# Kernel tuning notes

Hardware: AMD Instinct MI355X
Metric: run time of the kernel (lower is better)

The kernel has to match this reference:

```python
import jax, jax.numpy as jnp
import numpy as np

KS, STRIDE, PAD, GROUPS = 7, 1, 3, 8


def setup_inputs() -> dict:
    key = jax.random.key(0)
    ks = jax.random.split(key, 6)
    B, C, H, W = 4, 128, 64, 64
    O = 128
    rel_size = O // GROUPS // 2  # 8
    return {
        "x": jax.random.normal(ks[0], (B, C, H, W), jnp.float32),
        "wq": jax.random.normal(ks[1], (O, C), jnp.float32) * 0.05,
        "wk": jax.random.normal(ks[2], (O, C), jnp.float32) * 0.05,
        "wv": jax.random.normal(ks[3], (O, C), jnp.float32) * 0.05,
        "rel_x": jax.random.normal(ks[4], (rel_size, KS), jnp.float32),
        "rel_y": jax.random.normal(ks[5], (O // GROUPS - rel_size, KS), jnp.float32),
    }


def _patches(a, fH, fW):
    # a: [B, C, pH, pW] -> [B, C, fH, fW, KS, KS] (overlapping windows, like torch unfold)
    cols = []
    for ki in range(KS):
        rows = []
        for kj in range(KS):
            rows.append(a[:, :, ki:ki + (fH - 1) * STRIDE + 1:STRIDE,
                             kj:kj + (fW - 1) * STRIDE + 1:STRIDE])
        cols.append(jnp.stack(rows, axis=-1))  # last axis = l (W-kernel)
    return jnp.stack(cols, axis=-2)            # second-to-last = k (H-kernel)


def reference(x, wq, wk, wv, rel_x, rel_y):
    B, C, H, W = x.shape
    O = wq.shape[0]
    rel_size = rel_x.shape[0]
    xp = jnp.pad(x, ((0, 0), (0, 0), (PAD, PAD), (PAD, PAD)))
    pH, pW = H + 2 * PAD, W + 2 * PAD
    fH, fW = (pH - KS) // STRIDE + 1, (pW - KS) // STRIDE + 1
    # 1x1 convs
    q = jnp.einsum('oc,bchw->bohw', wq, xp)
    k = jnp.einsum('oc,bchw->bohw', wk, xp)
    v = jnp.einsum('oc,bchw->bohw', wv, xp)
    h0 = (KS - 1) // 2
    win_q = q[:, :, h0:pH - KS // 2:STRIDE, h0:pW - KS // 2:STRIDE]  # [B,O,fH,fW]
    win_q_b = win_q.reshape(B, GROUPS, O // GROUPS, fH, fW)
    qx = win_q_b[:, :, :rel_size]
    qy = win_q_b[:, :, rel_size:]
    bias_x = jnp.einsum('bgxhw,xk->bhwk', qx, rel_x)  # varies along l (W-kernel)
    bias_y = jnp.einsum('bgyhw,yk->bhwk', qy, rel_y)  # varies along k (H-kernel)
    win_k = _patches(k, fH, fW)  # [B,O,fH,fW,KS,KS]
    win_v = _patches(v, fH, fW)
    logits = jnp.einsum('bchw,bchwkl->bhwkl', win_q, win_k)
    logits = logits + bias_x[:, :, :, None, :] + bias_y[:, :, :, :, None]
    attn = jax.nn.softmax(logits.reshape(B, fH, fW, KS * KS), axis=-1)
    attn = attn.reshape(B, fH, fW, KS, KS)
    out = jnp.einsum('bhwkl,bchwkl->bchw', attn, win_v)  # [B,O,fH,fW]
    return out
```

## Files before the change

### kernel.cpp

```cpp
#include <hip/hip_runtime.h>

typedef __fp16 half8_t __attribute__((ext_vector_type(8)));
typedef __fp16 h2_t    __attribute__((ext_vector_type(2)));
typedef float  f4_t    __attribute__((ext_vector_type(4)));

constexpr int CI = 128, HW = 4096;

__device__ __forceinline__ h2_t u2h(unsigned u) { return __builtin_bit_cast(h2_t, u); }
__device__ __forceinline__ float dot2(unsigned k, unsigned q, float c) {
#if __has_builtin(__builtin_amdgcn_fdot2)
    return __builtin_amdgcn_fdot2(u2h(k), u2h(q), c, false);
#else
    h2_t kh = u2h(k), qh = u2h(q);
    return c + (float)kh[0] * (float)qh[0] + (float)kh[1] * (float)qh[1];
#endif
}

__global__ __launch_bounds__(256) void prepass(
    const float* __restrict__ x, const float* __restrict__ wq,
    const float* __restrict__ wk, const float* __restrict__ wv,
    __fp16* __restrict__ xh, __fp16* __restrict__ wh)
{
    const int tid = threadIdx.x, bx = blockIdx.x;
    const int wvn = tid >> 6, lane = tid & 63;
    const int quad = lane >> 4, n = lane & 15;
    if (bx < 1024) {
        const int t = bx, ck = wvn;
        const int p = t * 16 + n, b = p >> 12, hw = p & 4095;
        const float* src = x + (size_t)b * (CI * HW) + (size_t)(ck * 32 + quad * 8) * HW + hw;
        half8_t hv;
#pragma unroll
        for (int j = 0; j < 8; ++j) hv[j] = (__fp16)src[(size_t)j * HW];
        *(half8_t*)(xh + ((size_t)((t * 4 + ck) * 64 + lane)) * 8) = hv;
    } else {
        const int item = (bx - 1024) * 4 + wvn;
        const int g = item >> 3, ot = (item >> 2) & 1, ck = item & 3;
        const int mtx = g >> 2, olb = (g & 3) * 32;
        const float* wsrc = (mtx == 0) ? wq : (mtx == 1 ? wk : wv);
        const float* row = wsrc + (size_t)(olb + ot * 16 + n) * CI + ck * 32 + quad * 8;
        half8_t hv;
#pragma unroll
        for (int j = 0; j < 8; ++j) hv[j] = (__fp16)row[j];
        *(half8_t*)(wh + ((size_t)(item * 64 + lane)) * 8) = hv;
    }
}

__global__ __launch_bounds__(256) void qkv_mfma(
    const __fp16* __restrict__ xh, const __fp16* __restrict__ wh,
    unsigned* __restrict__ qf, unsigned* __restrict__ kf, unsigned* __restrict__ vf)
{
    __shared__ float tlds[4][16 * 17];
    const int tid = threadIdx.x, wvn = tid >> 6, lane = tid & 63;
    const int g = blockIdx.x;
    const int m = lane & 15, quad = lane >> 4;
    unsigned* dst = (g < 4) ? qf : (g < 8 ? kf : vf);
    const int c2base = (g & 3) * 16;

    half8_t A[2][4];
#pragma unroll
    for (int ot = 0; ot < 2; ++ot)
#pragma unroll
        for (int ck = 0; ck < 4; ++ck)
            A[ot][ck] = *(const half8_t*)(wh + ((size_t)((((g * 2 + ot) * 4 + ck) * 64 + lane)) * 8));

    float* tl = tlds[wvn];
    const int t0 = blockIdx.y * 16 + wvn * 4;
    for (int ti = 0; ti < 4; ++ti) {
        const int t = t0 + ti;
        half8_t B[4];
#pragma unroll
        for (int ck = 0; ck < 4; ++ck)
            B[ck] = *(const half8_t*)(xh + ((size_t)((t * 4 + ck) * 64 + lane)) * 8);
        const int p0 = t * 16;
#pragma unroll
        for (int ot = 0; ot < 2; ++ot) {
            f4_t acc = {0.f, 0.f, 0.f, 0.f};
#pragma unroll
            for (int ck = 0; ck < 4; ++ck)
                acc = __builtin_amdgcn_mfma_f32_16x16x32_f16(A[ot][ck], B[ck], acc, 0, 0, 0);
            const int c2l = ot * 8 + quad * 2;
            tl[m * 17 + c2l]     = __builtin_bit_cast(float, __builtin_amdgcn_cvt_pkrtz(acc[0], acc[1]));
            tl[m * 17 + c2l + 1] = __builtin_bit_cast(float, __builtin_amdgcn_cvt_pkrtz(acc[2], acc[3]));
        }
        __asm__ volatile("s_waitcnt lgkmcnt(0)" ::: "memory");
        __builtin_amdgcn_wave_barrier();
#pragma unroll
        for (int s = 0; s < 4; ++s) {
            const int px = s * 4 + quad, c2l = m;
            dst[(size_t)(p0 + px) * 64 + c2base + c2l] =
                __builtin_bit_cast(unsigned, tl[px * 17 + c2l]);
        }
        __builtin_amdgcn_wave_barrier();
    }
}

__global__ __launch_bounds__(512) void attn_kernel(
    const unsigned* __restrict__ qf, const unsigned* __restrict__ kf,
    const unsigned* __restrict__ vf, const float* __restrict__ relx,
    const float* __restrict__ rely, float* __restrict__ out)
{
    __shared__ unsigned smem[15232];
    unsigned* kS   = smem;
    unsigned* vS   = smem + 7296;
    float*    rels = (float*)(smem + 14592);
    float*    sxyL = (float*)(smem + 14704);
    float*    biasL= (float*)(smem + 14976);
    float*    otile= (float*)smem;

    const int tid = threadIdx.x, bx = blockIdx.x;
    const int wv = tid >> 6, lane = tid & 63;
    const int w0 = (bx & 7) * 8;
    const int h0 = ((bx >> 3) & 31) * 2;
    const int b  = bx >> 8;
    const int dr = wv >> 2, dw0 = (wv & 3) * 2;
    const int pixbase = b * 4096 + (h0 + dr) * 64 + (w0 + dw0);

    if (tid < 112) rels[tid] = (tid < 56) ? relx[tid] : rely[tid - 56];

#pragma unroll
    for (int it = 0; it < 14; ++it) {
        int idx = it * 512 + tid;
        const int isv = idx >= 3584;
        idx -= isv * 3584;
        const int pos = idx >> 5, c2 = (idx & 31) * 2;
        const int ri = pos / 14, ci = pos - ri * 14;
        const int r = h0 - 3 + ri, cw = w0 - 3 + ci;
        uint2 d = make_uint2(0u, 0u);
        if ((unsigned)r < 64u && (unsigned)cw < 64u) {
            const unsigned* src = isv ? vf : kf;
            d = *(const uint2*)(src + (size_t)((b * 4096 + r * 64 + cw) * 64 + c2));
        }
        unsigned* dstS = isv ? vS : kS;
        dstS[c2 * 114 + pos]       = d.x;
        dstS[(c2 + 1) * 114 + pos] = d.y;
    }

    if (lane < 32) {
        const int px01 = lane >> 4, t = lane & 15;
        const int pix = pixbase + px01;
        float s = 0.f;
#pragma unroll
        for (int gg = 0; gg < 8; ++gg) {
            const h2_t hh = u2h(qf[(size_t)pix * 64 + gg * 8 + (t >> 1)]);
            s += (float)hh[t & 1];
        }
        sxyL[(wv * 2 + px01) * 17 + t] = s;
    }
    __syncthreads();

    if (lane < 28) {
        const int px01 = lane >= 14;
        const int j = lane - px01 * 14;
        const int isy = j >= 7;
        const int jj = j - isy * 7;
        const float* sx = &sxyL[(wv * 2 + px01) * 17 + isy * 8];
        const float* rl = &rels[isy * 56 + jj];
        float s = 0.f;
#pragma unroll
        for (int i = 0; i < 8; ++i) s += sx[i] * rl[i * 7];
        biasL[(wv * 2 + px01) * 16 + j] = s;
    }
    __syncthreads();

    const int nn = (lane < 49) ? lane : 48;
    const int ki = (nn * 37) >> 8, kj = nn - ki * 7;
    int apk[2];
#pragma unroll
    for (int px01 = 0; px01 < 2; ++px01) {
        const int pixu = __builtin_amdgcn_readfirstlane(pixbase + px01);
        const uint4* qp = (const uint4*)(qf + (size_t)pixu * 64);
        const int pos = (dr + ki) * 14 + (dw0 + px01 + kj);
        float acc = 0.f;
#pragma unroll
        for (int c4 = 0; c4 < 16; ++c4) {
            const uint4 qw = qp[c4];
            acc = dot2(kS[(c4 * 4 + 0) * 114 + pos], qw.x, acc);
            acc = dot2(kS[(c4 * 4 + 1) * 114 + pos], qw.y, acc);
            acc = dot2(kS[(c4 * 4 + 2) * 114 + pos], qw.z, acc);
            acc = dot2(kS[(c4 * 4 + 3) * 114 + pos], qw.w, acc);
        }
        const float* bb = &biasL[(wv * 2 + px01) * 16];
        float logit = (lane < 49) ? acc + bb[kj] + bb[7 + ki] : -1e30f;
        float mx = logit;
#pragma unroll
        for (int off = 32; off; off >>= 1) mx = fmaxf(mx, __shfl_xor(mx, off));
        const float e = __expf(logit - mx);
        float ss = e;
#pragma unroll
        for (int off = 32; off; off >>= 1) ss += __shfl_xor(ss, off);
        const float a = e / ss;
        apk[px01] = __builtin_bit_cast(int, __builtin_amdgcn_cvt_pkrtz(a, a));
    }
    __syncthreads();

    const int posb = dr * 14 + dw0;
    h2_t o0 = {(__fp16)0.f, (__fp16)0.f}, o1 = o0;
#pragma unroll
    for (int n = 0; n < 49; ++n) {
        const int nki = (n * 37) >> 8, nkj = n - nki * 7;
        const int p = posb + nki * 14 + nkj;
        const unsigned va = vS[lane * 114 + p];
        const unsigned vb = vS[lane * 114 + p + 1];
        const h2_t a0 = u2h((unsigned)__builtin_amdgcn_readlane(apk[0], n));
        const h2_t a1 = u2h((unsigned)__builtin_amdgcn_readlane(apk[1], n));
        o0 += a0 * u2h(va);
        o1 += a1 * u2h(vb);
    }
    const int pxl0 = dr * 8 + dw0;
    {
        float2 f0 = make_float2((float)o0[0], (float)o0[1]);
        float2 f1 = make_float2((float)o1[0], (float)o1[1]);
        *(float2*)&otile[(size_t)pxl0 * 130 + lane * 2]       = f0;
        *(float2*)&otile[(size_t)(pxl0 + 1) * 130 + lane * 2] = f1;
    }
    __syncthreads();

#pragma unroll
    for (int s = 0; s < 4; ++s) {
        const int i = s * 512 + tid;
        const int c = i >> 4, pxl = i & 15;
        const int drr = pxl >> 3, dww = pxl & 7;
        out[(size_t)(b * 128 + c) * 4096 + (h0 + drr) * 64 + (w0 + dww)] =
            otile[pxl * 130 + c];
    }
}

extern "C" void kernel_launch(void* const* d_in, const int* in_sizes, int n_in,
                              void* d_out, int out_size, void* d_ws, size_t ws_size,
                              hipStream_t stream) {
    const float* x    = (const float*)d_in[0];
    const float* wq   = (const float*)d_in[1];
    const float* wk   = (const float*)d_in[2];
    const float* wv   = (const float*)d_in[3];
    const float* relx = (const float*)d_in[4];
    const float* rely = (const float*)d_in[5];
    float* out = (float*)d_out;

    char* ws = (char*)d_ws;
    __fp16*   xh = (__fp16*)(ws);
    __fp16*   wh = (__fp16*)(ws + 0x400000);
    unsigned* qf = (unsigned*)(ws + 0x420000);
    unsigned* kf = (unsigned*)(ws + 0x820000);
    unsigned* vf = (unsigned*)(ws + 0xC20000);

    prepass<<<dim3(1048), 256, 0, stream>>>(x, wq, wk, wv, xh, wh);
    qkv_mfma<<<dim3(12, 64), 256, 0, stream>>>(xh, wh, qf, kf, vf);
    attn_kernel<<<dim3(1024), 512, 0, stream>>>(qf, kf, vf, relx, rely, out);
}
```

Measured before the change: 106.1 us.

## Fuse fp16 conversion into QKV MFMA kernel and enlarge attention tiles

Removes the separate prepass that converted x and weights to fp16. The QKV projection kernel now converts weights into LDS and x into registers itself, and each block computes one full matrix for 64 pixels. The attention kernel moves to 1024-thread blocks covering 4x8 pixels, which shrinks the halo overhead of the K/V staging. It also interleaves the two pixels' dot products per wave. In exchange, each QKV block re-reads and re-converts the whole weight matrix, x is read three times (once per Q/K/V), and the larger LDS footprint may lower occupancy.

New measurement: 103.3 us. 2.6% less time.

```diff
diff --git a/kernel.cpp b/kernel.cpp
--- a/kernel.cpp
+++ b/kernel.cpp
@@ -3,8 +3,6 @@
 typedef __fp16 half8_t __attribute__((ext_vector_type(8)));
 typedef __fp16 h2_t    __attribute__((ext_vector_type(2)));
 typedef float  f4_t    __attribute__((ext_vector_type(4)));
-
-constexpr int CI = 128, HW = 4096;
 
 __device__ __forceinline__ h2_t u2h(unsigned u) { return __builtin_bit_cast(h2_t, u); }
 __device__ __forceinline__ float dot2(unsigned k, unsigned q, float c) {
@@ -15,114 +13,107 @@
     return c + (float)kh[0] * (float)qh[0] + (float)kh[1] * (float)qh[1];
 #endif
 }
-
-__global__ __launch_bounds__(256) void prepass(
+__device__ __forceinline__ unsigned pk(float a, float b) {
+    return __builtin_bit_cast(unsigned, __builtin_amdgcn_cvt_pkrtz(a, b));
+}
+
+__global__ __launch_bounds__(256) void qkv_fused(
     const float* __restrict__ x, const float* __restrict__ wq,
     const float* __restrict__ wk, const float* __restrict__ wv,
-    __fp16* __restrict__ xh, __fp16* __restrict__ wh)
+    unsigned* __restrict__ qf, unsigned* __restrict__ kf,
+    unsigned* __restrict__ vf)
 {
-    const int tid = threadIdx.x, bx = blockIdx.x;
-    const int wvn = tid >> 6, lane = tid & 63;
-    const int quad = lane >> 4, n = lane & 15;
-    if (bx < 1024) {
-        const int t = bx, ck = wvn;
-        const int p = t * 16 + n, b = p >> 12, hw = p & 4095;
-        const float* src = x + (size_t)b * (CI * HW) + (size_t)(ck * 32 + quad * 8) * HW + hw;
-        half8_t hv;
-#pragma unroll
-        for (int j = 0; j < 8; ++j) hv[j] = (__fp16)src[(size_t)j * HW];
-        *(half8_t*)(xh + ((size_t)((t * 4 + ck) * 64 + lane)) * 8) = hv;
-    } else {
-        const int item = (bx - 1024) * 4 + wvn;
-        const int g = item >> 3, ot = (item >> 2) & 1, ck = item & 3;
-        const int mtx = g >> 2, olb = (g & 3) * 32;
-        const float* wsrc = (mtx == 0) ? wq : (mtx == 1 ? wk : wv);
-        const float* row = wsrc + (size_t)(olb + ot * 16 + n) * CI + ck * 32 + quad * 8;
-        half8_t hv;
-#pragma unroll
-        for (int j = 0; j < 8; ++j) hv[j] = (__fp16)row[j];
-        *(half8_t*)(wh + ((size_t)(item * 64 + lane)) * 8) = hv;
-    }
-}
-
-__global__ __launch_bounds__(256) void qkv_mfma(
-    const __fp16* __restrict__ xh, const __fp16* __restrict__ wh,
-    unsigned* __restrict__ qf, unsigned* __restrict__ kf, unsigned* __restrict__ vf)
-{
-    __shared__ float tlds[4][16 * 17];
+    __shared__ __fp16 Af[2048 * 8];
+    __shared__ float  tl4[4][16 * 17];
+
     const int tid = threadIdx.x, wvn = tid >> 6, lane = tid & 63;
-    const int g = blockIdx.x;
+    const int mtx = blockIdx.x >> 8;
+    const int tg  = blockIdx.x & 255;
+    const float* wsrc = (mtx == 0) ? wq : (mtx == 1 ? wk : wv);
+    unsigned*    dst  = (mtx == 0) ? qf : (mtx == 1 ? kf : vf);
+
+#pragma unroll
+    for (int s = 0; s < 8; ++s) {
+        const int it = s * 256 + tid;
+        const int l = it & 63, ck = (it >> 6) & 3, ot = it >> 8;
+        const float* wr = wsrc + (size_t)(ot * 16 + (l & 15)) * 128 + ck * 32 + (l >> 4) * 8;
+        const float4 w0 = *(const float4*)wr;
+        const float4 w1 = *(const float4*)(wr + 4);
+        half8_t h;
+        h[0] = (__fp16)w0.x; h[1] = (__fp16)w0.y; h[2] = (__fp16)w0.z; h[3] = (__fp16)w0.w;
+        h[4] = (__fp16)w1.x; h[5] = (__fp16)w1.y; h[6] = (__fp16)w1.z; h[7] = (__fp16)w1.w;
+        *(half8_t*)&Af[it * 8] = h;
+    }
+
+    const int t = tg * 4 + wvn;
     const int m = lane & 15, quad = lane >> 4;
-    unsigned* dst = (g < 4) ? qf : (g < 8 ? kf : vf);
-    const int c2base = (g & 3) * 16;
-
-    half8_t A[2][4];
-#pragma unroll
-    for (int ot = 0; ot < 2; ++ot)
-#pragma unroll
-        for (int ck = 0; ck < 4; ++ck)
-            A[ot][ck] = *(const half8_t*)(wh + ((size_t)((((g * 2 + ot) * 4 + ck) * 64 + lane)) * 8));
-
-    float* tl = tlds[wvn];
-    const int t0 = blockIdx.y * 16 + wvn * 4;
-    for (int ti = 0; ti < 4; ++ti) {
-        const int t = t0 + ti;
-        half8_t B[4];
-#pragma unroll
-        for (int ck = 0; ck < 4; ++ck)
-            B[ck] = *(const half8_t*)(xh + ((size_t)((t * 4 + ck) * 64 + lane)) * 8);
-        const int p0 = t * 16;
+    const int p0 = t * 16, b = p0 >> 12, hw = p0 & 4095;
+    const float* xb = x + (size_t)b * (128 * 4096) + hw + m;
+    half8_t B[4];
+#pragma unroll
+    for (int ck = 0; ck < 4; ++ck) {
+        half8_t h;
+#pragma unroll
+        for (int j = 0; j < 8; ++j)
+            h[j] = (__fp16)xb[(size_t)(ck * 32 + quad * 8 + j) * 4096];
+        B[ck] = h;
+    }
+    __syncthreads();
+
+    float* tl = tl4[wvn];
+#pragma unroll
+    for (int og = 0; og < 4; ++og) {
 #pragma unroll
         for (int ot = 0; ot < 2; ++ot) {
+            const int otile = og * 2 + ot;
             f4_t acc = {0.f, 0.f, 0.f, 0.f};
 #pragma unroll
-            for (int ck = 0; ck < 4; ++ck)
-                acc = __builtin_amdgcn_mfma_f32_16x16x32_f16(A[ot][ck], B[ck], acc, 0, 0, 0);
+            for (int ck = 0; ck < 4; ++ck) {
+                const half8_t A = *(const half8_t*)&Af[((otile * 4 + ck) * 64 + lane) * 8];
+                acc = __builtin_amdgcn_mfma_f32_16x16x32_f16(A, B[ck], acc, 0, 0, 0);
+            }
             const int c2l = ot * 8 + quad * 2;
-            tl[m * 17 + c2l]     = __builtin_bit_cast(float, __builtin_amdgcn_cvt_pkrtz(acc[0], acc[1]));
-            tl[m * 17 + c2l + 1] = __builtin_bit_cast(float, __builtin_amdgcn_cvt_pkrtz(acc[2], acc[3]));
+            tl[m * 17 + c2l]     = __builtin_bit_cast(float, pk(acc[0], acc[1]));
+            tl[m * 17 + c2l + 1] = __builtin_bit_cast(float, pk(acc[2], acc[3]));
         }
         __asm__ volatile("s_waitcnt lgkmcnt(0)" ::: "memory");
         __builtin_amdgcn_wave_barrier();
 #pragma unroll
         for (int s = 0; s < 4; ++s) {
-            const int px = s * 4 + quad, c2l = m;
-            dst[(size_t)(p0 + px) * 64 + c2base + c2l] =
-                __builtin_bit_cast(unsigned, tl[px * 17 + c2l]);
+            const int px = s * 4 + quad;
+            dst[(size_t)(p0 + px) * 64 + og * 16 + m] =
+                __builtin_bit_cast(unsigned, tl[px * 17 + m]);
         }
         __builtin_amdgcn_wave_barrier();
     }
 }
 
-__global__ __launch_bounds__(512) void attn_kernel(
+__global__ __launch_bounds__(1024) void attn_kernel(
     const unsigned* __restrict__ qf, const unsigned* __restrict__ kf,
     const unsigned* __restrict__ vf, const float* __restrict__ relx,
     const float* __restrict__ rely, float* __restrict__ out)
 {
-    __shared__ unsigned smem[15232];
-    unsigned* kS   = smem;
-    unsigned* vS   = smem + 7296;
-    float*    rels = (float*)(smem + 14592);
-    float*    sxyL = (float*)(smem + 14704);
-    float*    biasL= (float*)(smem + 14976);
-    float*    otile= (float*)smem;
+    __shared__ unsigned smem[19472];
+    unsigned* kS    = smem;
+    unsigned* vS    = smem + 9152;
+    float*    rels  = (float*)(smem + 18304);
+    float*    sxyL  = (float*)(smem + 18416);
+    float*    biasL = (float*)(smem + 18960);
+    float*    otile = (float*)smem;
 
     const int tid = threadIdx.x, bx = blockIdx.x;
     const int wv = tid >> 6, lane = tid & 63;
     const int w0 = (bx & 7) * 8;
-    const int h0 = ((bx >> 3) & 31) * 2;
-    const int b  = bx >> 8;
+    const int h0 = ((bx >> 3) & 15) * 4;
+    const int b  = bx >> 7;
     const int dr = wv >> 2, dw0 = (wv & 3) * 2;
-    const int pixbase = b * 4096 + (h0 + dr) * 64 + (w0 + dw0);
 
     if (tid < 112) rels[tid] = (tid < 56) ? relx[tid] : rely[tid - 56];
 
-#pragma unroll
-    for (int it = 0; it < 14; ++it) {
-        int idx = it * 512 + tid;
-        const int isv = idx >= 3584;
-        idx -= isv * 3584;
-        const int pos = idx >> 5, c2 = (idx & 31) * 2;
+    for (int i = tid; i < 8960; i += 1024) {
+        const int isv = i >= 4480;
+        const int ii  = i - isv * 4480;
+        const int pos = ii >> 5, c2 = (ii & 31) * 2;
         const int ri = pos / 14, ci = pos - ri * 14;
         const int r = h0 - 3 + ri, cw = w0 - 3 + ci;
         uint2 d = make_uint2(0u, 0u);
@@ -131,56 +122,62 @@
             d = *(const uint2*)(src + (size_t)((b * 4096 + r * 64 + cw) * 64 + c2));
         }
         unsigned* dstS = isv ? vS : kS;
-        dstS[c2 * 114 + pos]       = d.x;
-        dstS[(c2 + 1) * 114 + pos] = d.y;
-    }
-
-    if (lane < 32) {
-        const int px01 = lane >> 4, t = lane & 15;
-        const int pix = pixbase + px01;
+        dstS[c2 * 143 + pos]       = d.x;
+        dstS[(c2 + 1) * 143 + pos] = d.y;
+    }
+
+    if (tid < 512) {
+        const int px = tid >> 4, tt = tid & 15;
+        const int pix = b * 4096 + (h0 + (px >> 3)) * 64 + w0 + (px & 7);
         float s = 0.f;
 #pragma unroll
-        for (int gg = 0; gg < 8; ++gg) {
-            const h2_t hh = u2h(qf[(size_t)pix * 64 + gg * 8 + (t >> 1)]);
-            s += (float)hh[t & 1];
-        }
-        sxyL[(wv * 2 + px01) * 17 + t] = s;
-    }
-    __syncthreads();
-
-    if (lane < 28) {
-        const int px01 = lane >= 14;
-        const int j = lane - px01 * 14;
-        const int isy = j >= 7;
-        const int jj = j - isy * 7;
-        const float* sx = &sxyL[(wv * 2 + px01) * 17 + isy * 8];
+        for (int g = 0; g < 8; ++g) {
+            const h2_t hh = u2h(qf[(size_t)pix * 64 + g * 8 + (tt >> 1)]);
+            s += (float)hh[tt & 1];
+        }
+        sxyL[px * 17 + tt] = s;
+    }
+    __syncthreads();
+
+    if (tid < 448) {
+        const int px = tid / 14, j = tid - px * 14;
+        const int isy = j >= 7, jj = j - isy * 7;
+        const float* sx = &sxyL[px * 17 + isy * 8];
         const float* rl = &rels[isy * 56 + jj];
         float s = 0.f;
 #pragma unroll
-        for (int i = 0; i < 8; ++i) s += sx[i] * rl[i * 7];
-        biasL[(wv * 2 + px01) * 16 + j] = s;
+        for (int i = 0; i < 8; ++i) s = fmaf(sx[i], rl[i * 7], s);
+        biasL[px * 16 + j] = s;
     }
     __syncthreads();
 
     const int nn = (lane < 49) ? lane : 48;
     const int ki = (nn * 37) >> 8, kj = nn - ki * 7;
-    int apk[2];
-#pragma unroll
-    for (int px01 = 0; px01 < 2; ++px01) {
-        const int pixu = __builtin_amdgcn_readfirstlane(pixbase + px01);
-        const uint4* qp = (const uint4*)(qf + (size_t)pixu * 64);
-        const int pos = (dr + ki) * 14 + (dw0 + px01 + kj);
-        float acc = 0.f;
-#pragma unroll
-        for (int c4 = 0; c4 < 16; ++c4) {
-            const uint4 qw = qp[c4];
-            acc = dot2(kS[(c4 * 4 + 0) * 114 + pos], qw.x, acc);
-            acc = dot2(kS[(c4 * 4 + 1) * 114 + pos], qw.y, acc);
-            acc = dot2(kS[(c4 * 4 + 2) * 114 + pos], qw.z, acc);
-            acc = dot2(kS[(c4 * 4 + 3) * 114 + pos], qw.w, acc);
-        }
-        const float* bb = &biasL[(wv * 2 + px01) * 16];
-        float logit = (lane < 49) ? acc + bb[kj] + bb[7 + ki] : -1e30f;
+    const int pixu = __builtin_amdgcn_readfirstlane(
+        b * 4096 + (h0 + dr) * 64 + (w0 + dw0));
+    const uint4* qp0 = (const uint4*)(qf + (size_t)pixu * 64);
+    const uint4* qp1 = (const uint4*)(qf + (size_t)(pixu + 1) * 64);
+    const int pos = (dr + ki) * 14 + (dw0 + kj);
+    float acc0 = 0.f, acc1 = 0.f;
+#pragma unroll
+    for (int c4 = 0; c4 < 16; ++c4) {
+        const uint4 q0 = qp0[c4], q1 = qp1[c4];
+        const unsigned* kb = &kS[(c4 * 4) * 143 + pos];
+        unsigned lo, hi;
+        lo = kb[0];       hi = kb[1];
+        acc0 = dot2(lo, q0.x, acc0); acc1 = dot2(hi, q1.x, acc1);
+        lo = kb[143];     hi = kb[144];
+        acc0 = dot2(lo, q0.y, acc0); acc1 = dot2(hi, q1.y, acc1);
+        lo = kb[286];     hi = kb[287];
+        acc0 = dot2(lo, q0.z, acc0); acc1 = dot2(hi, q1.z, acc1);
+        lo = kb[429];     hi = kb[430];
+        acc0 = dot2(lo, q0.w, acc0); acc1 = dot2(hi, q1.w, acc1);
+    }
+    const int pxl0 = dr * 8 + dw0;
+    int apk0, apk1;
+    {
+        const float* bb = &biasL[pxl0 * 16];
+        float logit = (lane < 49) ? acc0 + bb[kj] + bb[7 + ki] : -1e30f;
         float mx = logit;
 #pragma unroll
         for (int off = 32; off; off >>= 1) mx = fmaxf(mx, __shfl_xor(mx, off));
@@ -189,7 +186,20 @@
 #pragma unroll
         for (int off = 32; off; off >>= 1) ss += __shfl_xor(ss, off);
         const float a = e / ss;
-        apk[px01] = __builtin_bit_cast(int, __builtin_amdgcn_cvt_pkrtz(a, a));
+        apk0 = __builtin_bit_cast(int, __builtin_amdgcn_cvt_pkrtz(a, a));
+    }
+    {
+        const float* bb = &biasL[(pxl0 + 1) * 16];
+        float logit = (lane < 49) ? acc1 + bb[kj] + bb[7 + ki] : -1e30f;
+        float mx = logit;
+#pragma unroll
+        for (int off = 32; off; off >>= 1) mx = fmaxf(mx, __shfl_xor(mx, off));
+        const float e = __expf(logit - mx);
+        float ss = e;
+#pragma unroll
+        for (int off = 32; off; off >>= 1) ss += __shfl_xor(ss, off);
+        const float a = e / ss;
+        apk1 = __builtin_bit_cast(int, __builtin_amdgcn_cvt_pkrtz(a, a));
     }
     __syncthreads();
 
@@ -198,29 +208,24 @@
 #pragma unroll
     for (int n = 0; n < 49; ++n) {
         const int nki = (n * 37) >> 8, nkj = n - nki * 7;
-        const int p = posb + nki * 14 + nkj;
-        const unsigned va = vS[lane * 114 + p];
-        const unsigned vb = vS[lane * 114 + p + 1];
-        const h2_t a0 = u2h((unsigned)__builtin_amdgcn_readlane(apk[0], n));
-        const h2_t a1 = u2h((unsigned)__builtin_amdgcn_readlane(apk[1], n));
-        o0 += a0 * u2h(va);
-        o1 += a1 * u2h(vb);
-    }
-    const int pxl0 = dr * 8 + dw0;
-    {
-        float2 f0 = make_float2((float)o0[0], (float)o0[1]);
-        float2 f1 = make_float2((float)o1[0], (float)o1[1]);
-        *(float2*)&otile[(size_t)pxl0 * 130 + lane * 2]       = f0;
-        *(float2*)&otile[(size_t)(pxl0 + 1) * 130 + lane * 2] = f1;
-    }
+        const unsigned* vb = &vS[lane * 143 + posb + nki * 14 + nkj];
+        const unsigned lo = vb[0], hi = vb[1];
+        const h2_t a0 = u2h((unsigned)__builtin_amdgcn_readlane(apk0, n));
+        const h2_t a1 = u2h((unsigned)__builtin_amdgcn_readlane(apk1, n));
+        o0 += a0 * u2h(lo);
+        o1 += a1 * u2h(hi);
+    }
+    *(float2*)&otile[(size_t)pxl0 * 130 + lane * 2] =
+        make_float2((float)o0[0], (float)o0[1]);
+    *(float2*)&otile[(size_t)(pxl0 + 1) * 130 + lane * 2] =
+        make_float2((float)o1[0], (float)o1[1]);
     __syncthreads();
 
 #pragma unroll
     for (int s = 0; s < 4; ++s) {
-        const int i = s * 512 + tid;
-        const int c = i >> 4, pxl = i & 15;
-        const int drr = pxl >> 3, dww = pxl & 7;
-        out[(size_t)(b * 128 + c) * 4096 + (h0 + drr) * 64 + (w0 + dww)] =
+        const int i = s * 1024 + tid;
+        const int pxl = i & 31, c = i >> 5;
+        out[(size_t)(b * 128 + c) * 4096 + (h0 + (pxl >> 3)) * 64 + (w0 + (pxl & 7))] =
             otile[pxl * 130 + c];
     }
 }
@@ -237,13 +242,10 @@
     float* out = (float*)d_out;
 
     char* ws = (char*)d_ws;
-    __fp16*   xh = (__fp16*)(ws);
-    __fp16*   wh = (__fp16*)(ws + 0x400000);
-    unsigned* qf = (unsigned*)(ws + 0x420000);
-    unsigned* kf = (unsigned*)(ws + 0x820000);
-    unsigned* vf = (unsigned*)(ws + 0xC20000);
-
-    prepass<<<dim3(1048), 256, 0, stream>>>(x, wq, wk, wv, xh, wh);
-    qkv_mfma<<<dim3(12, 64), 256, 0, stream>>>(xh, wh, qf, kf, vf);
-    attn_kernel<<<dim3(1024), 512, 0, stream>>>(qf, kf, vf, relx, rely, out);
-}
+    unsigned* qfb = (unsigned*)(ws);
+    unsigned* kfb = (unsigned*)(ws + 0x400000);
+    unsigned* vfb = (unsigned*)(ws + 0x800000);
+
+    qkv_fused<<<dim3(768), 256, 0, stream>>>(x, wq, wk, wv, qfb, kfb, vfb);
+    attn_kernel<<<dim3(512), 1024, 0, stream>>>(qfb, kfb, vfb, relx, rely, out);
+}
```
